# Optimization experiments

Measured on AMD Instinct MI355X. Metric: run time of the kernel, lower is better.

The kernel has to match this reference:

```python
import jax, jax.numpy as jnp
import numpy as np

B, L, D_MODEL, H = 4, 2048, 1024, 16
HD = D_MODEL // H  # head_dim = 64


def _rope_tables(seq_len, dim, dtype):
    inv_freq = 1.0 / (10000.0 ** (jnp.arange(0, dim, 2, dtype=jnp.float32) / dim))
    t = jnp.arange(seq_len, dtype=jnp.float32)
    freqs = jnp.outer(t, inv_freq)  # (S, dim/2)
    return jnp.cos(freqs).astype(dtype), jnp.sin(freqs).astype(dtype)


def _apply_rope(x):
    # x: (B, H, S, d)
    cos, sin = _rope_tables(x.shape[-2], x.shape[-1], x.dtype)  # (S, d/2)
    x_even = x[..., 0::2]
    x_odd = x[..., 1::2]
    out_even = x_even * cos - x_odd * sin
    out_odd = x_even * sin + x_odd * cos
    return jnp.stack([out_even, out_odd], axis=-1).reshape(x.shape)


def setup_inputs() -> dict:
    key = jax.random.key(0)
    ks = jax.random.split(key, 9)
    s = 1.0 / np.sqrt(D_MODEL)
    inp = {
        "query": jax.random.normal(ks[0], (B, L, D_MODEL), dtype=jnp.float32),
        "Wq": jax.random.uniform(ks[1], (D_MODEL, D_MODEL), jnp.float32, -s, s),
        "bq": jax.random.uniform(ks[2], (D_MODEL,), jnp.float32, -s, s),
        "Wk": jax.random.uniform(ks[3], (D_MODEL, D_MODEL), jnp.float32, -s, s),
        "bk": jax.random.uniform(ks[4], (D_MODEL,), jnp.float32, -s, s),
        "Wv": jax.random.uniform(ks[5], (D_MODEL, D_MODEL), jnp.float32, -s, s),
        "bv": jax.random.uniform(ks[6], (D_MODEL,), jnp.float32, -s, s),
        "Wo": jax.random.uniform(ks[7], (D_MODEL, D_MODEL), jnp.float32, -s, s),
        "bo": jax.random.uniform(ks[8], (D_MODEL,), jnp.float32, -s, s),
    }
    return inp


def reference(query, Wq, bq, Wk, bk, Wv, bv, Wo, bo):
    Bq, Lq, _ = query.shape
    # projections (torch Linear: x @ W.T + b), split into heads -> (B, H, L, d)
    def proj(x, W, b):
        y = x @ W.T + b
        return y.reshape(Bq, Lq, H, HD).transpose(0, 2, 1, 3)
    q = _apply_rope(proj(query, Wq, bq))
    k = _apply_rope(proj(query, Wk, bk))
    v = proj(query, Wv, bv)
    scores = jnp.einsum("bhqd,bhkd->bhqk", q, k) / np.sqrt(HD)
    causal_mask = jnp.triu(jnp.ones((Lq, Lq), dtype=bool), k=1)
    scores = jnp.where(causal_mask[None, None, :, :], -jnp.inf, scores)
    attn = jax.nn.softmax(scores, axis=-1)
    out = jnp.einsum("bhqk,bhkd->bhqd", attn, v)
    out = out.transpose(0, 2, 1, 3).reshape(Bq, Lq, D_MODEL)
    return out @ Wo.T + bo
```

## Files before the change

### kernel.cpp

```cpp
#include <hip/hip_runtime.h>
#include <hip/hip_bf16.h>
#include <math.h>

#define L_SEQ  2048
#define DMODEL 1024
#define NHEAD  16
#define HEADD  64

typedef __attribute__((ext_vector_type(8))) short short8;
typedef __attribute__((ext_vector_type(4))) short short4v;
typedef __attribute__((ext_vector_type(4))) float f32x4;

static __device__ __forceinline__ unsigned short f2bf(float f) {
    unsigned int u = __float_as_uint(f);
    unsigned int r = (u + 0x7fffu + ((u >> 16) & 1u)) >> 16;
    return (unsigned short)r;
}

static __device__ __forceinline__ void dma16(const unsigned short* g, unsigned short* l) {
    __builtin_amdgcn_global_load_lds((const __attribute__((address_space(1))) void*)g,
                                     (__attribute__((address_space(3))) void*)l, 16, 0, 0);
}

__global__ __launch_bounds__(256) void prep(
    const float* __restrict__ query,
    const float* __restrict__ Wq, const float* __restrict__ Wk,
    const float* __restrict__ Wv, const float* __restrict__ Wo,
    unsigned short* __restrict__ xb, unsigned short* __restrict__ wdst,
    float* __restrict__ rope)
{
    int gid = blockIdx.x * 256 + threadIdx.x;
    if (gid < 2097152) {
        float4 v = reinterpret_cast<const float4*>(query)[gid];
        ushort4 o;
        o.x = f2bf(v.x); o.y = f2bf(v.y); o.z = f2bf(v.z); o.w = f2bf(v.w);
        reinterpret_cast<ushort4*>(xb)[gid] = o;
    } else if (gid < 2097152 + 1048576) {
        int i = gid - 2097152;
        int which = i >> 18;
        const float* src = which == 0 ? Wq : which == 1 ? Wk : which == 2 ? Wv : Wo;
        float4 v = reinterpret_cast<const float4*>(src)[i & 262143];
        ushort4 o;
        o.x = f2bf(v.x); o.y = f2bf(v.y); o.z = f2bf(v.z); o.w = f2bf(v.w);
        reinterpret_cast<ushort4*>(wdst)[i] = o;
    } else if (gid < 2097152 + 1048576 + 65536) {
        int i = gid - (2097152 + 1048576);
        int lpos = i >> 5, i2 = i & 31;
        float inv_f = expf(-0.28782313662425574f * (float)i2);
        float ang = (float)lpos * inv_f;
        rope[2 * i]     = cosf(ang);
        rope[2 * i + 1] = sinf(ang);
    }
}

#define BKP 32

__global__ __launch_bounds__(512, 4) void proj_qkv(
    const unsigned short* __restrict__ X,
    const unsigned short* __restrict__ Wqkv,
    const float* __restrict__ bq_,
    const float* __restrict__ bk_,
    const float* __restrict__ bv_,
    const float* __restrict__ rope,
    unsigned short* __restrict__ Qb,
    unsigned short* __restrict__ Kb,
    unsigned short* __restrict__ Vr)
{
    __shared__ unsigned short pool[36864];
    unsigned short* a_ring = pool;
    unsigned short* b_ring = pool + 12288;

    const int tid  = threadIdx.x;
    const int lane = tid & 63;
    const int w    = tid >> 6;
    const int wm   = w & 1, wn = w >> 1;
    const int quad = lane >> 4, l16 = lane & 15;

    const int orig = blockIdx.y * 12 + blockIdx.x;
    const int xcd  = orig & 7;
    const int k    = orig >> 3;
    const int by   = xcd * 8 + (k & 7);
    const int bxp  = k >> 3;
    const int m0   = by * 128;
    const int n0   = bxp * 256;

    const int sel = bxp >> 2;
    const float* bias   = sel == 0 ? bq_ : (sel == 1 ? bk_ : bv_);
    unsigned short* out = sel == 0 ? Qb  : (sel == 1 ? Kb  : Vr);

    const int st_row = lane >> 2;
    const int st_col = (((lane & 3) ^ ((lane >> 3) & 3)) << 3);
    const int rd = ((quad ^ ((l16 >> 1) & 3)) << 3);

    f32x4 acc[4][4];
#pragma unroll
    for (int i = 0; i < 4; ++i)
#pragma unroll
        for (int j = 0; j < 4; ++j) acc[i][j] = (f32x4){0.f, 0.f, 0.f, 0.f};

    const unsigned short* Xs = X    + (size_t)(m0 + w * 16 + st_row) * DMODEL + st_col;
    const unsigned short* Ws = Wqkv + (size_t)(n0 + w * 32 + st_row) * DMODEL + st_col;
    const int ldsA  = (w * 16) * BKP;
    const int ldsB0 = (w * 32) * BKP, ldsB1 = (w * 32 + 16) * BKP;

#pragma unroll
    for (int p = 0; p < 2; ++p) {
        const int kk = p * BKP;
        dma16(Xs + kk,               a_ring + p * 4096 + ldsA);
        dma16(Ws + kk,               b_ring + p * 8192 + ldsB0);
        dma16(Ws + 16 * DMODEL + kk, b_ring + p * 8192 + ldsB1);
    }
    asm volatile("s_waitcnt vmcnt(3)" ::: "memory");
    __builtin_amdgcn_s_barrier();

    for (int kt = 0; kt < 32; ++kt) {
        const int sA = (kt % 3) * 4096;
        const int sB = (kt % 3) * 8192;
        const int pA = ((kt + 2) % 3) * 4096;
        const int pB = ((kt + 2) % 3) * 8192;
        const int kk = ((kt + 2) & 31) * BKP;

        short8 af[4], bf[4];
#pragma unroll
        for (int i = 0; i < 4; ++i)
            af[i] = *reinterpret_cast<const short8*>(
                &a_ring[sA + (wm * 64 + i * 16 + l16) * BKP + rd]);
#pragma unroll
        for (int j = 0; j < 4; ++j)
            bf[j] = *reinterpret_cast<const short8*>(
                &b_ring[sB + (wn * 64 + j * 16 + l16) * BKP + rd]);
        dma16(Xs + kk,               a_ring + pA + ldsA);
        dma16(Ws + kk,               b_ring + pB + ldsB0);
        dma16(Ws + 16 * DMODEL + kk, b_ring + pB + ldsB1);
        __builtin_amdgcn_s_barrier();
        asm volatile("s_waitcnt lgkmcnt(0)" ::: "memory");
        __builtin_amdgcn_sched_barrier(0);
        __builtin_amdgcn_s_setprio(1);
#pragma unroll
        for (int i = 0; i < 4; ++i)
#pragma unroll
            for (int j = 0; j < 4; ++j)
                acc[i][j] = __builtin_amdgcn_mfma_f32_16x16x32_bf16(af[i], bf[j], acc[i][j], 0, 0, 0);
        __builtin_amdgcn_s_setprio(0);
        asm volatile("s_waitcnt vmcnt(3)" ::: "memory");
        __builtin_amdgcn_s_barrier();
    }
    asm volatile("s_waitcnt vmcnt(0)" ::: "memory");
    __builtin_amdgcn_s_barrier();

    const int b     = m0 >> 11;
    const int lpos0 = m0 & (L_SEQ - 1);
#pragma unroll
    for (int t = 0; t < 2; ++t) {
        if ((wn >> 1) == t) {
#pragma unroll
            for (int jf = 0; jf < 4; ++jf) {
                int nl = (wn & 1) * 64 + jf * 16 + l16;
                int nn = (bxp & 3) * 256 + t * 128 + nl;
                float bval = bias[nn];
                int d  = nn & (HEADD - 1);
                float sgn = (d & 1) ? 1.0f : -1.0f;
                int i2 = d >> 1;
#pragma unroll
                for (int mf = 0; mf < 4; ++mf) {
#pragma unroll
                    for (int r = 0; r < 4; ++r) {
                        int ml = wm * 64 + mf * 16 + quad * 4 + r;
                        int lpos = (m0 + ml) & (L_SEQ - 1);
                        float v = acc[mf][jf][r] + bval;
                        if (sel < 2) {
                            float p = __shfl_xor(v, 1);
                            float2 cs = *reinterpret_cast<const float2*>(&rope[(size_t)(lpos * 32 + i2) * 2]);
                            v = v * cs.x + sgn * cs.y * p;
                            if (sel == 0) v *= 0.18033688011112042f;
                        }
                        pool[(sel < 2) ? (ml * 136 + nl) : (nl * 136 + ml)] = f2bf(v);
                    }
                }
            }
        }
        asm volatile("s_waitcnt lgkmcnt(0)" ::: "memory");
        __builtin_amdgcn_s_barrier();
#pragma unroll
        for (int i = 0; i < 4; ++i) {
            int g   = i * 512 + tid;
            int row = g >> 4;
            int c8  = (g & 15) * 8;
            int4 val = *reinterpret_cast<const int4*>(&pool[row * 136 + c8]);
            size_t addr;
            if (sel < 2) {
                int n_g = (bxp & 3) * 256 + t * 128 + c8;
                int h = n_g >> 6, d = n_g & 63;
                addr = ((size_t)(b * NHEAD + h) * L_SEQ + (lpos0 + row)) * HEADD + d;
            } else {
                int n_g = (bxp & 3) * 256 + t * 128 + row;
                int h = n_g >> 6, d = n_g & 63;
                addr = ((size_t)(b * NHEAD + h) * HEADD + d) * L_SEQ + lpos0 + c8;
            }
            *reinterpret_cast<int4*>(out + addr) = val;
        }
        asm volatile("s_waitcnt lgkmcnt(0)" ::: "memory");
        __builtin_amdgcn_s_barrier();
    }
}

__global__ __launch_bounds__(256) void attn_fwd(
    const unsigned short* __restrict__ Q,
    const unsigned short* __restrict__ K,
    const unsigned short* __restrict__ Vt,
    unsigned short* __restrict__ Oa)
{
    __shared__ unsigned short k_lds[3][64 * 64];
    __shared__ unsigned short v_lds[3][64 * 64];
    const int tid  = threadIdx.x;
    const int lane = tid & 63;
    const int w    = tid >> 6;
    const int quad = lane >> 4, l16 = lane & 15;
    const int pair = blockIdx.y;
    const int bh   = blockIdx.x;
    const size_t base = (size_t)bh * L_SEQ * HEADD;
    const int b = bh >> 4, h = bh & 15;

    const int srow  = lane >> 3;
    const int sslot = lane & 7;
    const int ssw   = ((sslot ^ srow) << 3);
    const unsigned short* Ksrc = K  + base + (size_t)(w * 8 + srow) * HEADD + ssw;
    const unsigned short* Vsrc = Vt + base + (size_t)(w * 8 + srow) * L_SEQ + ssw;
    const int d0 = (w * 8) * 64;
    const int d1 = (32 + w * 8) * 64;
    const int swr = (l16 & 7);

    for (int half = 0; half < 2; ++half) {
        const int s = half ? (15 - pair) : pair;
        const int qrow0 = s * 128 + w * 16 + l16;
        const int qrow1 = qrow0 + 64;
        const int kbmax = 2 * s + 1;

        short8 qf0[2], qf1[2];
#pragma unroll
        for (int ks = 0; ks < 2; ++ks) {
            qf0[ks] = *reinterpret_cast<const short8*>(Q + base + (size_t)qrow0 * HEADD + ks * 32 + quad * 8);
            qf1[ks] = *reinterpret_cast<const short8*>(Q + base + (size_t)qrow1 * HEADD + ks * 32 + quad * 8);
        }

        f32x4 o0[4], o1[4];
#pragma unroll
        for (int nt = 0; nt < 4; ++nt) {
            o0[nt] = (f32x4){0.f, 0.f, 0.f, 0.f};
            o1[nt] = (f32x4){0.f, 0.f, 0.f, 0.f};
        }
        float lsum0 = 0.f, lsum1 = 0.f;

#pragma unroll
        for (int p = 0; p < 2; ++p) {
            dma16(Ksrc + (size_t)(p * 64) * HEADD,        &k_lds[p][d0]);
            dma16(Ksrc + (size_t)(p * 64 + 32) * HEADD,   &k_lds[p][d1]);
            dma16(Vsrc + p * 64,                          &v_lds[p][d0]);
            dma16(Vsrc + p * 64 + 32 * L_SEQ,             &v_lds[p][d1]);
        }
        asm volatile("s_waitcnt vmcnt(4)" ::: "memory");
        __builtin_amdgcn_s_barrier();

        for (int kb = 0; kb <= kbmax; ++kb) {
            const int slot = kb % 3;
            const int ps   = (kb + 2) % 3;
            const int kn   = (kb + 2) <= kbmax ? (kb + 2) : 0;
            dma16(Ksrc + (size_t)(kn * 64) * HEADD,        &k_lds[ps][d0]);
            dma16(Ksrc + (size_t)(kn * 64 + 32) * HEADD,   &k_lds[ps][d1]);
            dma16(Vsrc + kn * 64,                          &v_lds[ps][d0]);
            dma16(Vsrc + kn * 64 + 32 * L_SEQ,             &v_lds[ps][d1]);

            f32x4 st0[4], st1[4];
#pragma unroll
            for (int nt = 0; nt < 4; ++nt) {
                st0[nt] = (f32x4){0.f, 0.f, 0.f, 0.f};
                st1[nt] = (f32x4){0.f, 0.f, 0.f, 0.f};
            }
            __builtin_amdgcn_s_setprio(1);
#pragma unroll
            for (int ks = 0; ks < 2; ++ks)
#pragma unroll
                for (int nt = 0; nt < 4; ++nt) {
                    short8 kf = *reinterpret_cast<const short8*>(
                        &k_lds[slot][(nt * 16 + l16) * 64 + (((ks * 4 + quad) ^ swr) << 3)]);
                    st0[nt] = __builtin_amdgcn_mfma_f32_16x16x32_bf16(kf, qf0[ks], st0[nt], 0, 0, 0);
                    st1[nt] = __builtin_amdgcn_mfma_f32_16x16x32_bf16(kf, qf1[ks], st1[nt], 0, 0, 0);
                }
            __builtin_amdgcn_s_setprio(0);

            if (kb >= 2 * s) {
#pragma unroll
                for (int nt = 0; nt < 4; ++nt)
#pragma unroll
                    for (int r = 0; r < 4; ++r) {
                        int seqcol = kb * 64 + nt * 16 + quad * 4 + r;
                        if (seqcol > qrow0) st0[nt][r] = -INFINITY;
                    }
            }
            if (kb == kbmax) {
#pragma unroll
                for (int nt = 0; nt < 4; ++nt)
#pragma unroll
                    for (int r = 0; r < 4; ++r) {
                        int seqcol = kb * 64 + nt * 16 + quad * 4 + r;
                        if (seqcol > qrow1) st1[nt][r] = -INFINITY;
                    }
            }

            short4v pfrag0[4], pfrag1[4];
#pragma unroll
            for (int nt = 0; nt < 4; ++nt) {
                float p0 = __builtin_amdgcn_exp2f(st0[nt][0]);
                float p1 = __builtin_amdgcn_exp2f(st0[nt][1]);
                float p2 = __builtin_amdgcn_exp2f(st0[nt][2]);
                float p3 = __builtin_amdgcn_exp2f(st0[nt][3]);
                lsum0 += (p0 + p1) + (p2 + p3);
                unsigned u0 = __float_as_uint(p0) + 0x8000u;
                unsigned u1 = __float_as_uint(p1) + 0x8000u;
                unsigned u2 = __float_as_uint(p2) + 0x8000u;
                unsigned u3 = __float_as_uint(p3) + 0x8000u;
                union { unsigned u[2]; short4v v; } pk;
                pk.u[0] = (u0 >> 16) | (u1 & 0xffff0000u);
                pk.u[1] = (u2 >> 16) | (u3 & 0xffff0000u);
                pfrag0[nt] = pk.v;

                float q0e = __builtin_amdgcn_exp2f(st1[nt][0]);
                float q1e = __builtin_amdgcn_exp2f(st1[nt][1]);
                float q2e = __builtin_amdgcn_exp2f(st1[nt][2]);
                float q3e = __builtin_amdgcn_exp2f(st1[nt][3]);
                lsum1 += (q0e + q1e) + (q2e + q3e);
                unsigned v0 = __float_as_uint(q0e) + 0x8000u;
                unsigned v1 = __float_as_uint(q1e) + 0x8000u;
                unsigned v2 = __float_as_uint(q2e) + 0x8000u;
                unsigned v3 = __float_as_uint(q3e) + 0x8000u;
                union { unsigned u[2]; short4v v; } pk1;
                pk1.u[0] = (v0 >> 16) | (v1 & 0xffff0000u);
                pk1.u[1] = (v2 >> 16) | (v3 & 0xffff0000u);
                pfrag1[nt] = pk1.v;
            }

            __builtin_amdgcn_s_setprio(1);
#pragma unroll
            for (int c = 0; c < 4; ++c)
#pragma unroll
                for (int nt2 = 0; nt2 < 4; ++nt2) {
                    short4v vf = *reinterpret_cast<const short4v*>(
                        &v_lds[slot][(nt2 * 16 + l16) * 64 +
                                     (((c * 2 + (quad >> 1)) ^ swr) << 3) + ((quad & 1) << 2)]);
                    o0[nt2] = __builtin_amdgcn_mfma_f32_16x16x16bf16_1k(pfrag0[c], vf, o0[nt2], 0, 0, 0);
                    o1[nt2] = __builtin_amdgcn_mfma_f32_16x16x16bf16_1k(pfrag1[c], vf, o1[nt2], 0, 0, 0);
                }
            __builtin_amdgcn_s_setprio(0);

            asm volatile("s_waitcnt vmcnt(4)" ::: "memory");
            __builtin_amdgcn_s_barrier();
        }
        asm volatile("s_waitcnt vmcnt(0)" ::: "memory");
        __builtin_amdgcn_s_barrier();

        lsum0 += __shfl_xor(lsum0, 16);
        lsum0 += __shfl_xor(lsum0, 32);
        lsum1 += __shfl_xor(lsum1, 16);
        lsum1 += __shfl_xor(lsum1, 32);
        float rs0[4], rs1[4];
#pragma unroll
        for (int r = 0; r < 4; ++r) {
            rs0[r] = __shfl(lsum0, quad * 4 + r);
            rs1[r] = __shfl(lsum1, quad * 4 + r);
        }
#pragma unroll
        for (int r = 0; r < 4; ++r) {
            float inv0 = 1.0f / rs0[r];
            float inv1 = 1.0f / rs1[r];
            int lg0 = s * 128 + w * 16 + quad * 4 + r;
            int lg1 = lg0 + 64;
#pragma unroll
            for (int nt = 0; nt < 4; ++nt) {
                int d = nt * 16 + l16;
                Oa[(size_t)(b * L_SEQ + lg0) * DMODEL + h * HEADD + d] = f2bf(o0[nt][r] * inv0);
                Oa[(size_t)(b * L_SEQ + lg1) * DMODEL + h * HEADD + d] = f2bf(o1[nt][r] * inv1);
            }
        }
    }
}

__global__ __launch_bounds__(256) void out_gemm(
    const unsigned short* __restrict__ X,
    const unsigned short* __restrict__ W,
    const float* __restrict__ bias,
    float* __restrict__ out)
{
    __shared__ unsigned short a_lds[3][128 * BKP];
    __shared__ unsigned short b_lds[3][128 * BKP];
    const int tid  = threadIdx.x;
    const int lane = tid & 63;
    const int w    = tid >> 6;
    const int wm   = w & 1, wn = w >> 1;
    const int quad = lane >> 4, l16 = lane & 15;

    const int orig = blockIdx.y * 8 + blockIdx.x;
    const int xcd  = orig & 7;
    const int k    = orig >> 3;
    const int m0   = (xcd * 8 + (k & 7)) * 128;
    const int n0   = (k >> 3) * 128;

    const int st_row = lane >> 2;
    const int st_col = (((lane & 3) ^ ((lane >> 3) & 3)) << 3);
    const int rd = ((quad ^ ((l16 >> 1) & 3)) << 3);

    f32x4 acc[4][4];
#pragma unroll
    for (int i = 0; i < 4; ++i)
#pragma unroll
        for (int j = 0; j < 4; ++j) acc[i][j] = (f32x4){0.f, 0.f, 0.f, 0.f};

    const unsigned short* Xs = X + (size_t)(m0 + w * 32 + st_row) * DMODEL + st_col;
    const unsigned short* Ws = W + (size_t)(n0 + w * 32 + st_row) * DMODEL + st_col;
    const int ldsA0 = (w * 32) * BKP, ldsA1 = (w * 32 + 16) * BKP;

#pragma unroll
    for (int p = 0; p < 2; ++p) {
        const int kk = p * BKP;
        dma16(Xs + kk,               &a_lds[p][ldsA0]);
        dma16(Xs + 16 * DMODEL + kk, &a_lds[p][ldsA1]);
        dma16(Ws + kk,               &b_lds[p][ldsA0]);
        dma16(Ws + 16 * DMODEL + kk, &b_lds[p][ldsA1]);
    }
    asm volatile("s_waitcnt vmcnt(4)" ::: "memory");
    __builtin_amdgcn_s_barrier();

    for (int kt = 0; kt < 32; ++kt) {
        const int slot = kt % 3;
        const int ps   = (kt + 2) % 3;
        const int kk   = ((kt + 2) & 31) * BKP;

        dma16(Xs + kk,               &a_lds[ps][ldsA0]);
        dma16(Xs + 16 * DMODEL + kk, &a_lds[ps][ldsA1]);
        dma16(Ws + kk,               &b_lds[ps][ldsA0]);
        dma16(Ws + 16 * DMODEL + kk, &b_lds[ps][ldsA1]);

        short8 af[4], bf[4];
#pragma unroll
        for (int i = 0; i < 4; ++i)
            af[i] = *reinterpret_cast<const short8*>(
                &a_lds[slot][(wm * 64 + i * 16 + l16) * BKP + rd]);
#pragma unroll
        for (int j = 0; j < 4; ++j)
            bf[j] = *reinterpret_cast<const short8*>(
                &b_lds[slot][(wn * 64 + j * 16 + l16) * BKP + rd]);
        asm volatile("s_waitcnt lgkmcnt(0)" ::: "memory");
        __builtin_amdgcn_sched_barrier(0);
        __builtin_amdgcn_s_setprio(1);
#pragma unroll
        for (int i = 0; i < 4; ++i)
#pragma unroll
            for (int j = 0; j < 4; ++j)
                acc[i][j] = __builtin_amdgcn_mfma_f32_16x16x32_bf16(af[i], bf[j], acc[i][j], 0, 0, 0);
        __builtin_amdgcn_s_setprio(0);
        asm volatile("s_waitcnt vmcnt(4)" ::: "memory");
        __builtin_amdgcn_s_barrier();
    }
    asm volatile("s_waitcnt vmcnt(0)" ::: "memory");

#pragma unroll
    for (int nt = 0; nt < 4; ++nt) {
        int n_g = n0 + wn * 64 + nt * 16 + l16;
        float bv = bias[n_g];
#pragma unroll
        for (int mt = 0; mt < 4; ++mt)
#pragma unroll
            for (int r = 0; r < 4; ++r) {
                int m_g = m0 + wm * 64 + mt * 16 + quad * 4 + r;
                out[(size_t)m_g * DMODEL + n_g] = acc[mt][nt][r] + bv;
            }
    }
}

extern "C" void kernel_launch(void* const* d_in, const int* in_sizes, int n_in,
                              void* d_out, int out_size, void* d_ws, size_t ws_size,
                              hipStream_t stream) {
    const float* query = (const float*)d_in[0];
    const float* Wq = (const float*)d_in[1];
    const float* bq = (const float*)d_in[2];
    const float* Wk = (const float*)d_in[3];
    const float* bk = (const float*)d_in[4];
    const float* Wv = (const float*)d_in[5];
    const float* bv = (const float*)d_in[6];
    const float* Wo = (const float*)d_in[7];
    const float* bo = (const float*)d_in[8];
    float* out = (float*)d_out;

    unsigned short* ws  = (unsigned short*)d_ws;
    unsigned short* xb  = ws;
    unsigned short* wqb = xb  + (size_t)8388608;
    unsigned short* wkb = wqb + 1048576;
    unsigned short* wvb = wkb + 1048576;
    unsigned short* wob = wvb + 1048576;
    unsigned short* Qb  = wob + 1048576;
    unsigned short* Kb  = Qb  + 8388608;
    unsigned short* Vr  = Kb  + 8388608;
    unsigned short* Ab  = Vr  + 8388608;
    float* rope = (float*)(Ab + 8388608);

    (void)wkb; (void)wvb;

    prep<<<12545, 256, 0, stream>>>(query, Wq, Wk, Wv, Wo, xb, wqb, rope);

    proj_qkv<<<dim3(12, 64), 512, 0, stream>>>(xb, wqb, bq, bk, bv, rope, Qb, Kb, Vr);
    attn_fwd<<<dim3(64, 8), 256, 0, stream>>>(Qb, Kb, Vr, Ab);
    out_gemm<<<dim3(8, 64), 256, 0, stream>>>(Ab, wob, bo, out);
}
```

Measured before the change: 267.6 us.

## Widen out_gemm tile to 128x256 with 8 waves and shared LDS ring

The output projection GEMM moves from 256-thread blocks computing 128x128 tiles to 512-thread blocks computing 128x256 tiles, so each A tile in LDS feeds twice as many columns and the A-side global traffic is halved. The LDS buffers become one pool with a triple-buffered ring. DMA issue is moved after the fragment reads, with an extra barrier so the slot being overwritten is no longer in use. The larger tile halves the block count, which may reduce occupancy or load balance, and the extra barrier per k-step adds synchronisation cost.

Result: faster. 261.9 us (-2.1%).

```diff
diff --git a/kernel.cpp b/kernel.cpp
--- a/kernel.cpp
+++ b/kernel.cpp
@@ -384,25 +384,28 @@
     }
 }
 
-__global__ __launch_bounds__(256) void out_gemm(
+__global__ __launch_bounds__(512, 4) void out_gemm(
     const unsigned short* __restrict__ X,
     const unsigned short* __restrict__ W,
     const float* __restrict__ bias,
     float* __restrict__ out)
 {
-    __shared__ unsigned short a_lds[3][128 * BKP];
-    __shared__ unsigned short b_lds[3][128 * BKP];
+    __shared__ unsigned short pool[36864];
+    unsigned short* a_ring = pool;
+    unsigned short* b_ring = pool + 12288;
+
     const int tid  = threadIdx.x;
     const int lane = tid & 63;
     const int w    = tid >> 6;
     const int wm   = w & 1, wn = w >> 1;
     const int quad = lane >> 4, l16 = lane & 15;
 
-    const int orig = blockIdx.y * 8 + blockIdx.x;
+    const int orig = blockIdx.y * 4 + blockIdx.x;
     const int xcd  = orig & 7;
     const int k    = orig >> 3;
     const int m0   = (xcd * 8 + (k & 7)) * 128;
-    const int n0   = (k >> 3) * 128;
+    const int bxp  = k >> 3;
+    const int n0   = bxp * 256;
 
     const int st_row = lane >> 2;
     const int st_col = (((lane & 3) ^ ((lane >> 3) & 3)) << 3);
@@ -414,40 +417,41 @@
 #pragma unroll
         for (int j = 0; j < 4; ++j) acc[i][j] = (f32x4){0.f, 0.f, 0.f, 0.f};
 
-    const unsigned short* Xs = X + (size_t)(m0 + w * 32 + st_row) * DMODEL + st_col;
+    const unsigned short* Xs = X + (size_t)(m0 + w * 16 + st_row) * DMODEL + st_col;
     const unsigned short* Ws = W + (size_t)(n0 + w * 32 + st_row) * DMODEL + st_col;
-    const int ldsA0 = (w * 32) * BKP, ldsA1 = (w * 32 + 16) * BKP;
+    const int ldsA  = (w * 16) * BKP;
+    const int ldsB0 = (w * 32) * BKP, ldsB1 = (w * 32 + 16) * BKP;
 
 #pragma unroll
     for (int p = 0; p < 2; ++p) {
         const int kk = p * BKP;
-        dma16(Xs + kk,               &a_lds[p][ldsA0]);
-        dma16(Xs + 16 * DMODEL + kk, &a_lds[p][ldsA1]);
-        dma16(Ws + kk,               &b_lds[p][ldsA0]);
-        dma16(Ws + 16 * DMODEL + kk, &b_lds[p][ldsA1]);
-    }
-    asm volatile("s_waitcnt vmcnt(4)" ::: "memory");
+        dma16(Xs + kk,               a_ring + p * 4096 + ldsA);
+        dma16(Ws + kk,               b_ring + p * 8192 + ldsB0);
+        dma16(Ws + 16 * DMODEL + kk, b_ring + p * 8192 + ldsB1);
+    }
+    asm volatile("s_waitcnt vmcnt(3)" ::: "memory");
     __builtin_amdgcn_s_barrier();
 
     for (int kt = 0; kt < 32; ++kt) {
-        const int slot = kt % 3;
-        const int ps   = (kt + 2) % 3;
-        const int kk   = ((kt + 2) & 31) * BKP;
-
-        dma16(Xs + kk,               &a_lds[ps][ldsA0]);
-        dma16(Xs + 16 * DMODEL + kk, &a_lds[ps][ldsA1]);
-        dma16(Ws + kk,               &b_lds[ps][ldsA0]);
-        dma16(Ws + 16 * DMODEL + kk, &b_lds[ps][ldsA1]);
+        const int sA = (kt % 3) * 4096;
+        const int sB = (kt % 3) * 8192;
+        const int pA = ((kt + 2) % 3) * 4096;
+        const int pB = ((kt + 2) % 3) * 8192;
+        const int kk = ((kt + 2) & 31) * BKP;
 
         short8 af[4], bf[4];
 #pragma unroll
         for (int i = 0; i < 4; ++i)
             af[i] = *reinterpret_cast<const short8*>(
-                &a_lds[slot][(wm * 64 + i * 16 + l16) * BKP + rd]);
+                &a_ring[sA + (wm * 64 + i * 16 + l16) * BKP + rd]);
 #pragma unroll
         for (int j = 0; j < 4; ++j)
             bf[j] = *reinterpret_cast<const short8*>(
-                &b_lds[slot][(wn * 64 + j * 16 + l16) * BKP + rd]);
+                &b_ring[sB + (wn * 64 + j * 16 + l16) * BKP + rd]);
+        dma16(Xs + kk,               a_ring + pA + ldsA);
+        dma16(Ws + kk,               b_ring + pB + ldsB0);
+        dma16(Ws + 16 * DMODEL + kk, b_ring + pB + ldsB1);
+        __builtin_amdgcn_s_barrier();
         asm volatile("s_waitcnt lgkmcnt(0)" ::: "memory");
         __builtin_amdgcn_sched_barrier(0);
         __builtin_amdgcn_s_setprio(1);
@@ -457,7 +461,7 @@
             for (int j = 0; j < 4; ++j)
                 acc[i][j] = __builtin_amdgcn_mfma_f32_16x16x32_bf16(af[i], bf[j], acc[i][j], 0, 0, 0);
         __builtin_amdgcn_s_setprio(0);
-        asm volatile("s_waitcnt vmcnt(4)" ::: "memory");
+        asm volatile("s_waitcnt vmcnt(3)" ::: "memory");
         __builtin_amdgcn_s_barrier();
     }
     asm volatile("s_waitcnt vmcnt(0)" ::: "memory");
@@ -508,5 +512,5 @@
 
     proj_qkv<<<dim3(12, 64), 512, 0, stream>>>(xb, wqb, bq, bk, bv, rope, Qb, Kb, Vr);
     attn_fwd<<<dim3(64, 8), 256, 0, stream>>>(Qb, Kb, Vr, Ab);
-    out_gemm<<<dim3(8, 64), 256, 0, stream>>>(Ab, wob, bo, out);
-}
+    out_gemm<<<dim3(4, 64), 512, 0, stream>>>(Ab, wob, bo, out);
+}
```
